# Optimization experiments

Hardware: AMD Instinct MI355X
Metric: run time of the kernel (lower is better)

## Reference

```python
import jax, jax.numpy as jnp
import numpy as np

B, Q, K, C, H = 4, 1024, 1024, 1024, 16
L = C            # latent_dim (== in_dim per module construction)
CH = L // H      # head_dim = 64


def _ln(x, w, b):
    m = jnp.mean(x, -1, keepdims=True)
    v = jnp.mean((x - m) ** 2, -1, keepdims=True)
    return (x - m) * jax.lax.rsqrt(v + 1e-5) * w + b


def setup_inputs() -> dict:
    key = jax.random.key(0)
    ks = jax.random.split(key, 16)
    s = 0.02
    return {
        "queries": jax.random.normal(ks[0], (B, Q, C), jnp.float32),
        "contexts": jax.random.normal(ks[1], (B, K, C), jnp.float32),
        "queries_hidden": jax.random.normal(ks[2], (B, Q, L), jnp.float32),
        "sa_norm_w": jnp.ones((C,), jnp.float32),
        "sa_norm_b": jnp.zeros((C,), jnp.float32),
        "sa_qkv_w": jax.random.normal(ks[3], (C, 2 * L + C), jnp.float32) * s,
        "sa_out_w": jax.random.normal(ks[4], (C, C), jnp.float32) * s,
        "sa_out_b": jnp.zeros((C,), jnp.float32),
        "ca_norm_w": jnp.ones((C,), jnp.float32),
        "ca_norm_b": jnp.zeros((C,), jnp.float32),
        "gru_w_ih": jax.random.normal(ks[5], (3 * L, C), jnp.float32) * s,
        "gru_w_hh": jax.random.normal(ks[6], (3 * L, L), jnp.float32) * s,
        "gru_b_ih": jnp.zeros((3 * L,), jnp.float32),
        "gru_b_hh": jnp.zeros((3 * L,), jnp.float32),
        "ca_k_w": jax.random.normal(ks[7], (C, L), jnp.float32) * s,
        "ca_v_w": jax.random.normal(ks[8], (C, C), jnp.float32) * s,
        "ca_out_w": jax.random.normal(ks[9], (C, C), jnp.float32) * s,
        "ca_out_b": jnp.zeros((C,), jnp.float32),
        "ln1_w": jnp.ones((C,), jnp.float32),
        "ln1_b": jnp.zeros((C,), jnp.float32),
        "lin1_w": jax.random.normal(ks[10], (C, 2 * C), jnp.float32) * s,
        "ln2_w": jnp.ones((2 * C,), jnp.float32),
        "ln2_b": jnp.zeros((2 * C,), jnp.float32),
        "lin2_w": jax.random.normal(ks[11], (2 * C, C), jnp.float32) * s,
    }


def reference(queries, contexts, queries_hidden,
              sa_norm_w, sa_norm_b, sa_qkv_w, sa_out_w, sa_out_b,
              ca_norm_w, ca_norm_b, gru_w_ih, gru_w_hh, gru_b_ih, gru_b_hh,
              ca_k_w, ca_v_w, ca_out_w, ca_out_b,
              ln1_w, ln1_b, lin1_w, ln2_w, ln2_b, lin2_w):
    scale = 1.0 / jnp.sqrt(jnp.asarray(C, queries.dtype))

    # ---- SelfAttention (pre-norm, residual) ----
    xn = _ln(queries, sa_norm_w, sa_norm_b)
    qkv = (xn @ sa_qkv_w).reshape(B, Q, H, -1)          # [B,Q,H, 2*CH + C/H]
    q, k, v = jnp.split(qkv, [CH, 2 * CH], axis=-1)
    e = jnp.einsum('nqhc,nkhc->nhqk', q, k) * scale
    a = jax.nn.softmax(e, axis=-1)
    o = jnp.einsum('nhqk,nkhc->nqhc', a, v).reshape(B, Q, C)
    x = o @ sa_out_w + sa_out_b + queries

    # ---- AttentionDynamicQuery (GRU-updated queries, cross-attn) ----
    x_pre = x
    xn = _ln(x, ca_norm_w, ca_norm_b)
    xf = xn.reshape(B * Q, C)
    hf = queries_hidden.reshape(B * Q, L)
    gi = xf @ gru_w_ih.T + gru_b_ih                     # [BQ, 3L]
    gh = hf @ gru_w_hh.T + gru_b_hh
    gir, giz, gin = jnp.split(gi, 3, axis=-1)
    ghr, ghz, ghn = jnp.split(gh, 3, axis=-1)
    r = jax.nn.sigmoid(gir + ghr)
    z = jax.nn.sigmoid(giz + ghz)
    n = jnp.tanh(gin + r * ghn)
    h = (1.0 - z) * n + z * hf                          # PyTorch GRUCell update
    qh = h.reshape(B, Q, H, CH)                         # new queries_hidden

    kk = (contexts @ ca_k_w).reshape(B, K, H, CH)
    vv = (contexts @ ca_v_w).reshape(B, K, H, C // H)
    energy = jnp.einsum('nqhc,nkhc->nhqk', qh, kk)      # returned UNscaled
    att = jax.nn.softmax(energy * scale, axis=-1)
    o = jnp.einsum('nhqk,nkhc->nqhc', att, vv).reshape(B, Q, C)
    x = o @ ca_out_w + ca_out_b + x_pre

    # ---- MLP: LN -> SiLU -> Linear -> LN -> SiLU -> Linear, residual ----
    m = jax.nn.silu(_ln(x, ln1_w, ln1_b)) @ lin1_w
    m = jax.nn.silu(_ln(m, ln2_w, ln2_b)) @ lin2_w
    out = x + m                                         # dropout(p=0) = identity
    return (out, energy, qh)
```

## Files before the change

kernel.cpp:

```cpp
#include <hip/hip_runtime.h>
#include <hip/hip_bf16.h>
#include <math.h>

static constexpr float SCALE = 0.03125f;

typedef __attribute__((ext_vector_type(4))) float f32x4;
typedef __attribute__((ext_vector_type(8))) __bf16 bf16x8;
typedef __attribute__((ext_vector_type(4))) __bf16 bf16x4;

__device__ __forceinline__ void g2l16(const void* g, void* l) {
  __builtin_amdgcn_global_load_lds(
      (const __attribute__((address_space(1))) unsigned int*)g,
      (__attribute__((address_space(3))) unsigned int*)l,
      16, 0, 0);
}

__global__ __launch_bounds__(256) void prep_all(
    const float* __restrict__ sa_qkv_w, const float* __restrict__ ca_k_w,
    const float* __restrict__ ca_v_w, const float* __restrict__ sa_out_w,
    const float* __restrict__ ca_out_w, const float* __restrict__ lin1_w,
    const float* __restrict__ lin2_w, const float* __restrict__ gru_w_ih,
    const float* __restrict__ gru_w_hh, const float* __restrict__ qhid,
    const float* __restrict__ contexts,
    __bf16* __restrict__ qkvT, __bf16* __restrict__ kT, __bf16* __restrict__ vT,
    __bf16* __restrict__ saoT, __bf16* __restrict__ caoT, __bf16* __restrict__ lin1T,
    __bf16* __restrict__ lin2T, __bf16* __restrict__ ihB, __bf16* __restrict__ hhB,
    __bf16* __restrict__ qhB, __bf16* __restrict__ ctxB) {
  int bid = blockIdx.x;
  int t = threadIdx.x;
  if (bid >= 2816) {
    const float* csrc; __bf16* cdst; int cbase;
    if (bid < 4352)      { csrc = gru_w_ih; cdst = ihB;  cbase = 2816; }
    else if (bid < 5888) { csrc = gru_w_hh; cdst = hhB;  cbase = 4352; }
    else if (bid < 7936) { csrc = qhid;     cdst = qhB;  cbase = 5888; }
    else                 { csrc = contexts; cdst = ctxB; cbase = 7936; }
    size_t idx = ((size_t)(bid - cbase) * 256 + t) * 8;
    float4 a = *(const float4*)(csrc + idx);
    float4 b = *(const float4*)(csrc + idx + 4);
    bf16x8 o = {(__bf16)a.x,(__bf16)a.y,(__bf16)a.z,(__bf16)a.w,
                (__bf16)b.x,(__bf16)b.y,(__bf16)b.z,(__bf16)b.w};
    *(bf16x8*)(cdst + idx) = o;
    return;
  }
  const float* src; __bf16* dst; int Kd, N, base;
  if (bid < 768)       { src = sa_qkv_w; dst = qkvT;  Kd = 1024; N = 3072; base = 0; }
  else if (bid < 1024) { src = ca_k_w;   dst = kT;    Kd = 1024; N = 1024; base = 768; }
  else if (bid < 1280) { src = ca_v_w;   dst = vT;    Kd = 1024; N = 1024; base = 1024; }
  else if (bid < 1536) { src = sa_out_w; dst = saoT;  Kd = 1024; N = 1024; base = 1280; }
  else if (bid < 1792) { src = ca_out_w; dst = caoT;  Kd = 1024; N = 1024; base = 1536; }
  else if (bid < 2304) { src = lin1_w;   dst = lin1T; Kd = 1024; N = 2048; base = 1792; }
  else                 { src = lin2_w;   dst = lin2T; Kd = 2048; N = 1024; base = 2304; }
  int tid = bid - base;
  int ntx = N >> 6;
  int n0 = (tid % ntx) * 64, k0 = (tid / ntx) * 64;
  __shared__ float tile[64][65];
  #pragma unroll
  for (int i = 0; i < 16; ++i) {
    int idx = i * 256 + t; int r = idx >> 6, c = idx & 63;
    tile[r][c] = src[(size_t)(k0 + r) * N + n0 + c];
  }
  __syncthreads();
  #pragma unroll
  for (int i = 0; i < 16; ++i) {
    int idx = i * 256 + t; int r = idx >> 6, c = idx & 63;
    dst[(size_t)(n0 + r) * Kd + k0 + c] = (__bf16)tile[c][r];
  }
}

template <int NV>
__global__ __launch_bounds__(256) void ln_bf16(
    const float* __restrict__ xf, const __bf16* __restrict__ xb,
    const float* __restrict__ w, const float* __restrict__ b,
    __bf16* __restrict__ out, int silu) {
  const int D = NV * 1024;
  int row = blockIdx.x, t = threadIdx.x;
  float vals[NV * 4];
  float s = 0.f, s2 = 0.f;
  #pragma unroll
  for (int i = 0; i < NV; ++i) {
    int c = (i * 256 + t) * 4;
    float4 v;
    if (xf) {
      v = *(const float4*)(xf + (size_t)row * D + c);
    } else {
      bf16x4 vb = *(const bf16x4*)(xb + (size_t)row * D + c);
      v = make_float4((float)vb[0], (float)vb[1], (float)vb[2], (float)vb[3]);
    }
    vals[i*4+0] = v.x; vals[i*4+1] = v.y; vals[i*4+2] = v.z; vals[i*4+3] = v.w;
    s += v.x + v.y + v.z + v.w;
    s2 += v.x*v.x + v.y*v.y + v.z*v.z + v.w*v.w;
  }
  __shared__ float red[256], red2[256];
  red[t] = s; red2[t] = s2;
  __syncthreads();
  for (int off = 128; off > 0; off >>= 1) {
    if (t < off) { red[t] += red[t + off]; red2[t] += red2[t + off]; }
    __syncthreads();
  }
  float mean = red[0] / D;
  float var = red2[0] / D - mean * mean;
  float rs = rsqrtf(var + 1e-5f);
  #pragma unroll
  for (int i = 0; i < NV; ++i) {
    int c = (i * 256 + t) * 4;
    bf16x4 o;
    #pragma unroll
    for (int j = 0; j < 4; ++j) {
      float v = (vals[i*4+j] - mean) * rs * w[c+j] + b[c+j];
      if (silu) v = v / (1.f + __expf(-v));
      o[j] = (__bf16)v;
    }
    *(bf16x4*)(out + (size_t)row * D + c) = o;
  }
}

__global__ __launch_bounds__(256) void gemm_bf16(
    const __bf16* __restrict__ A, long long lda,
    const __bf16* __restrict__ B, long long ldb,
    float* __restrict__ outF, __bf16* __restrict__ outB, long long ldc,
    const float* __restrict__ bias, const float* __restrict__ res, int K) {
  __shared__ __bf16 Asm[128 * 64];
  __shared__ __bf16 Bsm[128 * 64];
  int nwg = gridDim.x * gridDim.y;
  int orig = blockIdx.y * gridDim.x + blockIdx.x;
  int swz = (orig & 7) * (nwg >> 3) + (orig >> 3);
  int bm = (swz / gridDim.x) * 128, bn = (swz % gridDim.x) * 128;
  int t = threadIdx.x;
  int lane = t & 63, w = t >> 6;
  int l15 = lane & 15, kg = lane >> 4;
  int wm = (w >> 1) * 64, wn = (w & 1) * 64;

  f32x4 acc[4][4];
  #pragma unroll
  for (int i = 0; i < 4; ++i)
    #pragma unroll
    for (int j = 0; j < 4; ++j) acc[i][j] = (f32x4)(0.0f);

  const __bf16* ga[4]; const __bf16* gb[4];
  __bf16* la[4]; __bf16* lb[4];
  #pragma unroll
  for (int i = 0; i < 4; ++i) {
    int slot = i * 256 + t;
    int row = slot >> 3, s = slot & 7;
    int sx = s ^ (row & 7);
    ga[i] = A + (size_t)(bm + row) * lda + (sx << 3);
    gb[i] = B + (size_t)(bn + row) * ldb + (sx << 3);
    int base = (i * 256 + w * 64) << 3;
    la[i] = Asm + base;
    lb[i] = Bsm + base;
  }

  for (int k0 = 0; k0 < K; k0 += 64) {
    #pragma unroll
    for (int i = 0; i < 4; ++i) g2l16(ga[i] + k0, la[i]);
    #pragma unroll
    for (int i = 0; i < 4; ++i) g2l16(gb[i] + k0, lb[i]);
    asm volatile("s_waitcnt vmcnt(0)" ::: "memory");
    __syncthreads();
    #pragma unroll
    for (int kk = 0; kk < 2; ++kk) {
      bf16x8 af[4], bfr[4];
      #pragma unroll
      for (int mi = 0; mi < 4; ++mi) {
        int row = wm + mi * 16 + l15;
        int ks = kk * 4 + kg;
        af[mi] = *(const bf16x8*)(Asm + row * 64 + ((ks ^ (row & 7)) << 3));
      }
      #pragma unroll
      for (int ni = 0; ni < 4; ++ni) {
        int row = wn + ni * 16 + l15;
        int ks = kk * 4 + kg;
        bfr[ni] = *(const bf16x8*)(Bsm + row * 64 + ((ks ^ (row & 7)) << 3));
      }
      #pragma unroll
      for (int mi = 0; mi < 4; ++mi)
        #pragma unroll
        for (int ni = 0; ni < 4; ++ni)
          acc[mi][ni] = __builtin_amdgcn_mfma_f32_16x16x32_bf16(
              af[mi], bfr[ni], acc[mi][ni], 0, 0, 0);
    }
    __syncthreads();
  }

  #pragma unroll
  for (int mi = 0; mi < 4; ++mi) {
    #pragma unroll
    for (int ni = 0; ni < 4; ++ni) {
      int rbase = bm + wm + mi * 16 + kg * 4;
      int c = bn + wn + ni * 16 + l15;
      #pragma unroll
      for (int r = 0; r < 4; ++r) {
        float val = acc[mi][ni][r];
        if (bias) val += bias[c];
        size_t off = (size_t)(rbase + r) * ldc + c;
        if (res) val += res[off];
        if (outF) outF[off] = val;
        if (outB) outB[off] = (__bf16)val;
      }
    }
  }
}

__global__ __launch_bounds__(256) void vtrans(
    const __bf16* __restrict__ V, long long v_sb, long long v_sh, int v_sm,
    __bf16* __restrict__ VT) {
  __shared__ __bf16 tile[64][72];
  int g = blockIdx.y, b = g >> 4, h = g & 15;
  int k0 = blockIdx.x * 64;
  const __bf16* Vb = V + (size_t)b * v_sb + (size_t)h * v_sh;
  int t = threadIdx.x;
  #pragma unroll
  for (int i = 0; i < 2; ++i) {
    int idx = i * 256 + t;
    int k = idx >> 3, dc = (idx & 7) * 8;
    bf16x8 v = *(const bf16x8*)(Vb + (size_t)(k0 + k) * v_sm + dc);
    #pragma unroll
    for (int j = 0; j < 8; ++j) tile[dc + j][k] = v[j];
  }
  __syncthreads();
  #pragma unroll
  for (int i = 0; i < 2; ++i) {
    int idx = i * 256 + t;
    int d = idx >> 3, kc = (idx & 7) * 8;
    bf16x8 v;
    #pragma unroll
    for (int j = 0; j < 8; ++j) v[j] = tile[d][kc + j];
    *(bf16x8*)(VT + ((size_t)g * 64 + d) * 1024 + k0 + kc) = v;
  }
}

__global__ __launch_bounds__(256) void flash_attn(
    const __bf16* __restrict__ Qb, long long q_sb, long long q_sh, int q_sm,
    const __bf16* __restrict__ Kb, long long k_sb, long long k_sh, int k_sm,
    const __bf16* __restrict__ VT, __bf16* __restrict__ Ob,
    float* __restrict__ energyOut, float scale) {
  __shared__ __bf16 Ksm[64 * 64];
  __shared__ __bf16 Vsm[64 * 64];
  __shared__ __bf16 Psm[128 * 64];
  __shared__ float corr_l[128];
  __shared__ float l_l[128];
  int g = blockIdx.y, b = g >> 4, h = g & 15;
  int qt = blockIdx.x * 128;
  const __bf16* Qg = Qb + (size_t)b * q_sb + (size_t)h * q_sh;
  const __bf16* Kg = Kb + (size_t)b * k_sb + (size_t)h * k_sh;
  const __bf16* Vg = VT + (size_t)g * 65536;
  int t = threadIdx.x, lane = t & 63, w = t >> 6;
  int l15 = lane & 15, kg = lane >> 4;
  int wq = w * 32;

  bf16x8 qf[2][2];
  #pragma unroll
  for (int nq = 0; nq < 2; ++nq)
    #pragma unroll
    for (int kk = 0; kk < 2; ++kk)
      qf[nq][kk] = *(const bf16x8*)(
          Qg + (size_t)(qt + wq + nq * 16 + l15) * q_sm + kk * 32 + kg * 8);

  f32x4 acc_o[2][4];
  #pragma unroll
  for (int i = 0; i < 2; ++i)
    #pragma unroll
    for (int j = 0; j < 4; ++j) acc_o[i][j] = (f32x4)(0.0f);
  float m_run[2] = {-1e30f, -1e30f};
  float l_run[2] = {0.f, 0.f};

  const __bf16* gK[2]; const __bf16* gV[2];
  __bf16 *lK[2], *lV[2];
  #pragma unroll
  for (int i = 0; i < 2; ++i) {
    int slot = i * 256 + t;
    int row = slot >> 3, s = slot & 7, sx = s ^ (row & 7);
    gK[i] = Kg + (size_t)row * k_sm + (sx << 3);
    gV[i] = Vg + (size_t)row * 1024 + (sx << 3);
    lK[i] = Ksm + ((i * 256 + w * 64) << 3);
    lV[i] = Vsm + ((i * 256 + w * 64) << 3);
  }

  for (int kv0 = 0; kv0 < 1024; kv0 += 64) {
    #pragma unroll
    for (int i = 0; i < 2; ++i) g2l16(gK[i] + (size_t)kv0 * k_sm, lK[i]);
    #pragma unroll
    for (int i = 0; i < 2; ++i) g2l16(gV[i] + kv0, lV[i]);
    asm volatile("s_waitcnt vmcnt(0)" ::: "memory");
    __syncthreads();

    f32x4 accs[4][2];
    #pragma unroll
    for (int i = 0; i < 4; ++i)
      #pragma unroll
      for (int j = 0; j < 2; ++j) accs[i][j] = (f32x4)(0.0f);
    #pragma unroll
    for (int tt = 0; tt < 4; ++tt) {
      bf16x8 kf[2];
      #pragma unroll
      for (int kk = 0; kk < 2; ++kk) {
        int row = tt * 16 + l15;
        int ks = kk * 4 + kg;
        kf[kk] = *(const bf16x8*)(Ksm + row * 64 + ((ks ^ (row & 7)) << 3));
      }
      #pragma unroll
      for (int nq = 0; nq < 2; ++nq)
        #pragma unroll
        for (int kk = 0; kk < 2; ++kk)
          accs[tt][nq] = __builtin_amdgcn_mfma_f32_16x16x32_bf16(
              kf[kk], qf[nq][kk], accs[tt][nq], 0, 0, 0);
    }

    if (energyOut) {
      float* eg = energyOut + ((size_t)g << 20);
      #pragma unroll
      for (int nq = 0; nq < 2; ++nq) {
        int q = qt + wq + nq * 16 + l15;
        #pragma unroll
        for (int tt = 0; tt < 4; ++tt)
          *(f32x4*)(eg + (size_t)q * 1024 + kv0 + tt * 16 + kg * 4) = accs[tt][nq];
      }
    }

    #pragma unroll
    for (int nq = 0; nq < 2; ++nq) {
      float tmax = -1e30f;
      #pragma unroll
      for (int tt = 0; tt < 4; ++tt)
        #pragma unroll
        for (int r = 0; r < 4; ++r) tmax = fmaxf(tmax, accs[tt][nq][r]);
      tmax *= scale;
      tmax = fmaxf(tmax, __shfl_xor(tmax, 16));
      tmax = fmaxf(tmax, __shfl_xor(tmax, 32));
      float m_new = fmaxf(m_run[nq], tmax);
      float corr = __expf(m_run[nq] - m_new);
      m_run[nq] = m_new;
      int q = wq + nq * 16 + l15;
      float psum = 0.f;
      #pragma unroll
      for (int tt = 0; tt < 4; ++tt) {
        bf16x4 p4;
        #pragma unroll
        for (int r = 0; r < 4; ++r) {
          float p = __expf(accs[tt][nq][r] * scale - m_new);
          psum += p;
          p4[r] = (__bf16)p;
        }
        int kvs = (tt * 16 + kg * 4) ^ ((q & 7) << 3);
        *(bf16x4*)(Psm + q * 64 + kvs) = p4;
      }
      psum += __shfl_xor(psum, 16);
      psum += __shfl_xor(psum, 32);
      l_run[nq] = l_run[nq] * corr + psum;
      if (kg == 0) corr_l[q] = corr;
    }
    __syncthreads();

    #pragma unroll
    for (int mq = 0; mq < 2; ++mq) {
      f32x4 c4 = *(const f32x4*)&corr_l[wq + mq * 16 + kg * 4];
      #pragma unroll
      for (int nd = 0; nd < 4; ++nd)
        #pragma unroll
        for (int r = 0; r < 4; ++r) acc_o[mq][nd][r] *= c4[r];
    }
    #pragma unroll
    for (int kk = 0; kk < 2; ++kk) {
      bf16x8 pf[2], vf[4];
      #pragma unroll
      for (int mq = 0; mq < 2; ++mq) {
        int row = wq + mq * 16 + l15;
        int kvs = (kk * 32 + kg * 8) ^ ((row & 7) << 3);
        pf[mq] = *(const bf16x8*)(Psm + row * 64 + kvs);
      }
      #pragma unroll
      for (int nd = 0; nd < 4; ++nd) {
        int vrow = nd * 16 + l15;
        vf[nd] = *(const bf16x8*)(Vsm + vrow * 64 + (((kk * 4 + kg) ^ (vrow & 7)) << 3));
      }
      #pragma unroll
      for (int mq = 0; mq < 2; ++mq)
        #pragma unroll
        for (int nd = 0; nd < 4; ++nd)
          acc_o[mq][nd] = __builtin_amdgcn_mfma_f32_16x16x32_bf16(
              pf[mq], vf[nd], acc_o[mq][nd], 0, 0, 0);
    }
    __syncthreads();
  }

  #pragma unroll
  for (int nq = 0; nq < 2; ++nq)
    if (kg == 0) l_l[wq + nq * 16 + l15] = l_run[nq];
  __syncthreads();

  #pragma unroll
  for (int mq = 0; mq < 2; ++mq) {
    f32x4 lv = *(const f32x4*)&l_l[wq + mq * 16 + kg * 4];
    #pragma unroll
    for (int nd = 0; nd < 4; ++nd) {
      int col = h * 64 + nd * 16 + l15;
      #pragma unroll
      for (int r = 0; r < 4; ++r) {
        int qrow = qt + wq + mq * 16 + kg * 4 + r;
        Ob[(size_t)(b * 1024 + qrow) * 1024 + col] = (__bf16)(acc_o[mq][nd][r] / lv[r]);
      }
    }
  }
}

__global__ __launch_bounds__(256) void gru_kernel(
    const __bf16* __restrict__ gi, const __bf16* __restrict__ gh,
    const float* __restrict__ hf, float* __restrict__ qh, __bf16* __restrict__ qhb) {
  size_t e0 = ((size_t)blockIdx.x * 256 + threadIdx.x) * 8;
  int row = (int)(e0 >> 10), col = (int)(e0 & 1023);
  size_t base = (size_t)row * 3072 + col;
  bf16x8 vir = *(const bf16x8*)(gi + base);
  bf16x8 viz = *(const bf16x8*)(gi + base + 1024);
  bf16x8 vin = *(const bf16x8*)(gi + base + 2048);
  bf16x8 vhr = *(const bf16x8*)(gh + base);
  bf16x8 vhz = *(const bf16x8*)(gh + base + 1024);
  bf16x8 vhn = *(const bf16x8*)(gh + base + 2048);
  float4 h0 = *(const float4*)(hf + e0);
  float4 h1 = *(const float4*)(hf + e0 + 4);
  float hv[8] = {h0.x, h0.y, h0.z, h0.w, h1.x, h1.y, h1.z, h1.w};
  float q[8];
  #pragma unroll
  for (int j = 0; j < 8; ++j) {
    float r = 1.f / (1.f + __expf(-((float)vir[j] + (float)vhr[j])));
    float z = 1.f / (1.f + __expf(-((float)viz[j] + (float)vhz[j])));
    float n = tanhf((float)vin[j] + r * (float)vhn[j]);
    q[j] = (1.f - z) * n + z * hv[j];
  }
  *(float4*)(qh + e0)     = make_float4(q[0], q[1], q[2], q[3]);
  *(float4*)(qh + e0 + 4) = make_float4(q[4], q[5], q[6], q[7]);
  bf16x8 qb;
  #pragma unroll
  for (int j = 0; j < 8; ++j) qb[j] = (__bf16)q[j];
  *(bf16x8*)(qhb + e0) = qb;
}

extern "C" void kernel_launch(void* const* d_in, const int* in_sizes, int n_in,
                              void* d_out, int out_size, void* d_ws, size_t ws_size,
                              hipStream_t stream) {
  (void)in_sizes; (void)n_in; (void)out_size; (void)ws_size;
  const float* queries   = (const float*)d_in[0];
  const float* contexts  = (const float*)d_in[1];
  const float* qhid      = (const float*)d_in[2];
  const float* sa_norm_w = (const float*)d_in[3];
  const float* sa_norm_b = (const float*)d_in[4];
  const float* sa_qkv_w  = (const float*)d_in[5];
  const float* sa_out_w  = (const float*)d_in[6];
  const float* sa_out_b  = (const float*)d_in[7];
  const float* ca_norm_w = (const float*)d_in[8];
  const float* ca_norm_b = (const float*)d_in[9];
  const float* gru_w_ih  = (const float*)d_in[10];
  const float* gru_w_hh  = (const float*)d_in[11];
  const float* gru_b_ih  = (const float*)d_in[12];
  const float* gru_b_hh  = (const float*)d_in[13];
  const float* ca_k_w    = (const float*)d_in[14];
  const float* ca_v_w    = (const float*)d_in[15];
  const float* ca_out_w  = (const float*)d_in[16];
  const float* ca_out_b  = (const float*)d_in[17];
  const float* ln1_w     = (const float*)d_in[18];
  const float* ln1_b     = (const float*)d_in[19];
  const float* lin1_w    = (const float*)d_in[20];
  const float* ln2_w     = (const float*)d_in[21];
  const float* ln2_b     = (const float*)d_in[22];
  const float* lin2_w    = (const float*)d_in[23];

  float* out0   = (float*)d_out;
  float* energy = out0 + (size_t)4194304;
  float* qh_out = out0 + (size_t)71303168;

  const size_t MM = 1u << 20;
  float* ws = (float*)d_ws;
  float*  X     = ws;
  float*  X2    = ws + 4 * MM;
  __bf16* M1B    = (__bf16*)(ws + 9 * MM);
  __bf16* XN_b   = (__bf16*)(ws + 17 * MM);
  __bf16* QHID_b = (__bf16*)(ws + 19 * MM);
  __bf16* CTX_b  = (__bf16*)(ws + 21 * MM);
  __bf16* O_b    = (__bf16*)(ws + 23 * MM);
  __bf16* VT_b   = (__bf16*)(ws + 25 * MM);
  __bf16* QKV_b  = (__bf16*)(ws + 27 * MM);
  __bf16* KV_b   = (__bf16*)(ws + 27 * MM);
  __bf16* LN2_b  = (__bf16*)(ws);
  __bf16* qkvT   = (__bf16*)(ws + 33 * MM);
  __bf16* ihB    = (__bf16*)(ws + 34 * MM + MM / 2);
  __bf16* hhB    = (__bf16*)(ws + 36 * MM);
  __bf16* kT     = (__bf16*)(ws + 37 * MM + MM / 2);
  __bf16* vT     = (__bf16*)(ws + 38 * MM);
  __bf16* saoT   = (__bf16*)(ws + 38 * MM + MM / 2);
  __bf16* caoT   = (__bf16*)(ws + 39 * MM);
  __bf16* lin1T  = (__bf16*)(ws + 39 * MM + MM / 2);
  __bf16* lin2T  = (__bf16*)(ws + 40 * MM + MM / 2);
  __bf16* GI_b = (__bf16*)energy;
  __bf16* GH_b = (__bf16*)(energy + 6 * MM);

  const long long QKV_SB = 1024LL * 3072;
  const long long KV_SB  = 1024LL * 2048;

  prep_all<<<9984, 256, 0, stream>>>(
      sa_qkv_w, ca_k_w, ca_v_w, sa_out_w, ca_out_w, lin1_w, lin2_w,
      gru_w_ih, gru_w_hh, qhid, contexts,
      qkvT, kT, vT, saoT, caoT, lin1T, lin2T, ihB, hhB, QHID_b, CTX_b);

  ln_bf16<1><<<4096, 256, 0, stream>>>(queries, nullptr, sa_norm_w, sa_norm_b, XN_b, 0);
  gemm_bf16<<<dim3(24, 32), 256, 0, stream>>>(
      XN_b, 1024, qkvT, 1024, nullptr, QKV_b, 3072, nullptr, nullptr, 1024);
  vtrans<<<dim3(16, 64), 256, 0, stream>>>(QKV_b + 128, QKV_SB, 192, 3072, VT_b);
  flash_attn<<<dim3(8, 64), 256, 0, stream>>>(
      QKV_b, QKV_SB, 192, 3072, QKV_b + 64, QKV_SB, 192, 3072,
      VT_b, O_b, nullptr, SCALE);
  gemm_bf16<<<dim3(8, 32), 256, 0, stream>>>(
      O_b, 1024, saoT, 1024, X, nullptr, 1024, sa_out_b, queries, 1024);

  ln_bf16<1><<<4096, 256, 0, stream>>>(X, nullptr, ca_norm_w, ca_norm_b, XN_b, 0);
  gemm_bf16<<<dim3(24, 32), 256, 0, stream>>>(
      XN_b, 1024, ihB, 1024, nullptr, GI_b, 3072, gru_b_ih, nullptr, 1024);
  gemm_bf16<<<dim3(24, 32), 256, 0, stream>>>(
      QHID_b, 1024, hhB, 1024, nullptr, GH_b, 3072, gru_b_hh, nullptr, 1024);
  gru_kernel<<<2048, 256, 0, stream>>>(GI_b, GH_b, qhid, qh_out, QHID_b );

  gemm_bf16<<<dim3(16, 32), 256, 0, stream>>>(
      CTX_b, 1024, kT, 1024, nullptr, KV_b, 2048, nullptr, nullptr, 1024);
  vtrans<<<dim3(16, 64), 256, 0, stream>>>(KV_b + 1024, KV_SB, 64, 2048, VT_b);
  flash_attn<<<dim3(8, 64), 256, 0, stream>>>(
      QHID_b, 1024LL * 1024, 64, 1024, KV_b, KV_SB, 64, 2048,
      VT_b, O_b, energy, SCALE);
  gemm_bf16<<<dim3(8, 32), 256, 0, stream>>>(
      O_b, 1024, caoT, 1024, X2, nullptr, 1024, ca_out_b, X, 1024);

  ln_bf16<1><<<4096, 256, 0, stream>>>(X2, nullptr, ln1_w, ln1_b, XN_b, 1);
  gemm_bf16<<<dim3(16, 32), 256, 0, stream>>>(
      XN_b, 1024, lin1T, 1024, nullptr, M1B, 2048, nullptr, nullptr, 1024);
  ln_bf16<2><<<4096, 256, 0, stream>>>(nullptr, M1B, ln2_w, ln2_b, LN2_b, 1);
  gemm_bf16<<<dim3(8, 32), 256, 0, stream>>>(
      LN2_b, 2048, lin2T, 2048, out0, nullptr, 1024, nullptr, X2, 2048);
}
```

Before: 654.0 us.

## Triple-buffer flash attention K/V, merge independent GEMMs, and use shuffle reductions in LN

Flash attention now prefetches K/V tiles two steps ahead into a three-slot LDS ring, using counted vmcnt waits and a single barrier per step in place of full drains. It also raises wave priority around the MFMA sections and writes the energy output with nontemporal stores. Independent GEMMs (sa_out with gru_hh, gru_ih with the context K/V projection) are merged into one dual-problem launch to fill the GPU and cut launch count. LayerNorm switches its reduction from a shared-memory tree to wave shuffles. The vmcnt counts are hand-tuned to the issue order, so any change in how loads are issued could break correctness.

```diff
diff --git a/kernel.cpp b/kernel.cpp
--- a/kernel.cpp
+++ b/kernel.cpp
@@ -90,15 +90,19 @@
     s += v.x + v.y + v.z + v.w;
     s2 += v.x*v.x + v.y*v.y + v.z*v.z + v.w*v.w;
   }
-  __shared__ float red[256], red2[256];
-  red[t] = s; red2[t] = s2;
+  #pragma unroll
+  for (int off = 32; off > 0; off >>= 1) {
+    s += __shfl_xor(s, off);
+    s2 += __shfl_xor(s2, off);
+  }
+  __shared__ float red[4], red2[4];
+  int wv = t >> 6;
+  if ((t & 63) == 0) { red[wv] = s; red2[wv] = s2; }
   __syncthreads();
-  for (int off = 128; off > 0; off >>= 1) {
-    if (t < off) { red[t] += red[t + off]; red2[t] += red2[t + off]; }
-    __syncthreads();
-  }
-  float mean = red[0] / D;
-  float var = red2[0] / D - mean * mean;
+  float S  = red[0] + red[1] + red[2] + red[3];
+  float S2 = red2[0] + red2[1] + red2[2] + red2[3];
+  float mean = S / D;
+  float var = S2 / D - mean * mean;
   float rs = rsqrtf(var + 1e-5f);
   #pragma unroll
   for (int i = 0; i < NV; ++i) {
@@ -114,17 +118,13 @@
   }
 }
 
-__global__ __launch_bounds__(256) void gemm_bf16(
+__device__ __forceinline__ void gemm_body(
+    __bf16* Asm, __bf16* Bsm,
     const __bf16* __restrict__ A, long long lda,
     const __bf16* __restrict__ B, long long ldb,
     float* __restrict__ outF, __bf16* __restrict__ outB, long long ldc,
-    const float* __restrict__ bias, const float* __restrict__ res, int K) {
-  __shared__ __bf16 Asm[128 * 64];
-  __shared__ __bf16 Bsm[128 * 64];
-  int nwg = gridDim.x * gridDim.y;
-  int orig = blockIdx.y * gridDim.x + blockIdx.x;
-  int swz = (orig & 7) * (nwg >> 3) + (orig >> 3);
-  int bm = (swz / gridDim.x) * 128, bn = (swz % gridDim.x) * 128;
+    const float* __restrict__ bias, const float* __restrict__ res,
+    int K, int bm, int bn) {
   int t = threadIdx.x;
   int lane = t & 63, w = t >> 6;
   int l15 = lane & 15, kg = lane >> 4;
@@ -201,6 +201,41 @@
   }
 }
 
+__global__ __launch_bounds__(256) void gemm_bf16(
+    const __bf16* __restrict__ A, long long lda,
+    const __bf16* __restrict__ B, long long ldb,
+    float* __restrict__ outF, __bf16* __restrict__ outB, long long ldc,
+    const float* __restrict__ bias, const float* __restrict__ res, int K) {
+  __shared__ __bf16 sm[2 * 8192];
+  int nwg = gridDim.x * gridDim.y;
+  int orig = blockIdx.y * gridDim.x + blockIdx.x;
+  int swz = (orig & 7) * (nwg >> 3) + (orig >> 3);
+  gemm_body(sm, sm + 8192, A, lda, B, ldb, outF, outB, ldc, bias, res, K,
+            (swz / gridDim.x) * 128, (swz % gridDim.x) * 128);
+}
+
+__global__ __launch_bounds__(256) void gemm_dual(
+    const __bf16* __restrict__ A0, long long lda0, const __bf16* __restrict__ B0, long long ldb0,
+    float* __restrict__ oF0, __bf16* __restrict__ oB0, long long ldc0,
+    const float* __restrict__ bias0, const float* __restrict__ res0, int K0, int gx0, int nb0,
+    const __bf16* __restrict__ A1, long long lda1, const __bf16* __restrict__ B1, long long ldb1,
+    float* __restrict__ oF1, __bf16* __restrict__ oB1, long long ldc1,
+    const float* __restrict__ bias1, const float* __restrict__ res1, int K1, int gx1) {
+  __shared__ __bf16 sm[2 * 8192];
+  int bid = blockIdx.x;
+  if (bid < nb0) {
+    int swz = (bid & 7) * (nb0 >> 3) + (bid >> 3);
+    gemm_body(sm, sm + 8192, A0, lda0, B0, ldb0, oF0, oB0, ldc0, bias0, res0, K0,
+              (swz / gx0) * 128, (swz % gx0) * 128);
+  } else {
+    int b = bid - nb0;
+    int nb1 = gridDim.x - nb0;
+    int swz = (b & 7) * (nb1 >> 3) + (b >> 3);
+    gemm_body(sm, sm + 8192, A1, lda1, B1, ldb1, oF1, oB1, ldc1, bias1, res1, K1,
+              (swz / gx1) * 128, (swz % gx1) * 128);
+  }
+}
+
 __global__ __launch_bounds__(256) void vtrans(
     const __bf16* __restrict__ V, long long v_sb, long long v_sh, int v_sm,
     __bf16* __restrict__ VT) {
@@ -229,13 +264,14 @@
   }
 }
 
+template <int E>
 __global__ __launch_bounds__(256) void flash_attn(
     const __bf16* __restrict__ Qb, long long q_sb, long long q_sh, int q_sm,
     const __bf16* __restrict__ Kb, long long k_sb, long long k_sh, int k_sm,
     const __bf16* __restrict__ VT, __bf16* __restrict__ Ob,
     float* __restrict__ energyOut, float scale) {
-  __shared__ __bf16 Ksm[64 * 64];
-  __shared__ __bf16 Vsm[64 * 64];
+  __shared__ __bf16 Ksm[3][4096];
+  __shared__ __bf16 Vsm[3][4096];
   __shared__ __bf16 Psm[128 * 64];
   __shared__ float corr_l[128];
   __shared__ float l_l[128];
@@ -265,30 +301,56 @@
   float l_run[2] = {0.f, 0.f};
 
   const __bf16* gK[2]; const __bf16* gV[2];
-  __bf16 *lK[2], *lV[2];
+  int lo[2];
   #pragma unroll
   for (int i = 0; i < 2; ++i) {
     int slot = i * 256 + t;
     int row = slot >> 3, s = slot & 7, sx = s ^ (row & 7);
     gK[i] = Kg + (size_t)row * k_sm + (sx << 3);
     gV[i] = Vg + (size_t)row * 1024 + (sx << 3);
-    lK[i] = Ksm + ((i * 256 + w * 64) << 3);
-    lV[i] = Vsm + ((i * 256 + w * 64) << 3);
-  }
-
-  for (int kv0 = 0; kv0 < 1024; kv0 += 64) {
-    #pragma unroll
-    for (int i = 0; i < 2; ++i) g2l16(gK[i] + (size_t)kv0 * k_sm, lK[i]);
-    #pragma unroll
-    for (int i = 0; i < 2; ++i) g2l16(gV[i] + kv0, lV[i]);
-    asm volatile("s_waitcnt vmcnt(0)" ::: "memory");
-    __syncthreads();
+    lo[i] = (i * 256 + w * 64) << 3;
+  }
+
+  #pragma unroll
+  for (int i = 0; i < 2; ++i) g2l16(gK[i], &Ksm[0][lo[i]]);
+  #pragma unroll
+  for (int i = 0; i < 2; ++i) g2l16(gV[i], &Vsm[0][lo[i]]);
+  #pragma unroll
+  for (int i = 0; i < 2; ++i) g2l16(gK[i] + (size_t)64 * k_sm, &Ksm[1][lo[i]]);
+  #pragma unroll
+  for (int i = 0; i < 2; ++i) g2l16(gV[i] + 64, &Vsm[1][lo[i]]);
+
+  int rb = 0;
+  for (int kvt = 0; kvt < 16; ++kvt) {
+    if (E) {
+      if (kvt == 0)       asm volatile("s_waitcnt vmcnt(4)" ::: "memory");
+      else if (kvt == 1)  asm volatile("s_waitcnt vmcnt(12)" ::: "memory");
+      else if (kvt == 15) asm volatile("s_waitcnt vmcnt(16)" ::: "memory");
+      else                asm volatile("s_waitcnt vmcnt(20)" ::: "memory");
+    } else {
+      if (kvt == 15)      asm volatile("s_waitcnt vmcnt(0)" ::: "memory");
+      else                asm volatile("s_waitcnt vmcnt(4)" ::: "memory");
+    }
+    __builtin_amdgcn_s_barrier();
+    __builtin_amdgcn_sched_barrier(0);
+
+    if (kvt < 14) {
+      int sbuf = rb >= 1 ? rb - 1 : rb + 2;
+      size_t ko = (size_t)(kvt + 2) << 6;
+      #pragma unroll
+      for (int i = 0; i < 2; ++i) g2l16(gK[i] + ko * k_sm, &Ksm[sbuf][lo[i]]);
+      #pragma unroll
+      for (int i = 0; i < 2; ++i) g2l16(gV[i] + ko, &Vsm[sbuf][lo[i]]);
+    }
+    const __bf16* Ks = Ksm[rb];
+    const __bf16* Vs = Vsm[rb];
 
     f32x4 accs[4][2];
     #pragma unroll
     for (int i = 0; i < 4; ++i)
       #pragma unroll
       for (int j = 0; j < 2; ++j) accs[i][j] = (f32x4)(0.0f);
+    __builtin_amdgcn_s_setprio(1);
     #pragma unroll
     for (int tt = 0; tt < 4; ++tt) {
       bf16x8 kf[2];
@@ -296,7 +358,7 @@
       for (int kk = 0; kk < 2; ++kk) {
         int row = tt * 16 + l15;
         int ks = kk * 4 + kg;
-        kf[kk] = *(const bf16x8*)(Ksm + row * 64 + ((ks ^ (row & 7)) << 3));
+        kf[kk] = *(const bf16x8*)(Ks + row * 64 + ((ks ^ (row & 7)) << 3));
       }
       #pragma unroll
       for (int nq = 0; nq < 2; ++nq)
@@ -305,15 +367,18 @@
           accs[tt][nq] = __builtin_amdgcn_mfma_f32_16x16x32_bf16(
               kf[kk], qf[nq][kk], accs[tt][nq], 0, 0, 0);
     }
-
-    if (energyOut) {
+    __builtin_amdgcn_s_setprio(0);
+
+    if (E) {
+      int kv0 = kvt << 6;
       float* eg = energyOut + ((size_t)g << 20);
       #pragma unroll
       for (int nq = 0; nq < 2; ++nq) {
         int q = qt + wq + nq * 16 + l15;
         #pragma unroll
         for (int tt = 0; tt < 4; ++tt)
-          *(f32x4*)(eg + (size_t)q * 1024 + kv0 + tt * 16 + kg * 4) = accs[tt][nq];
+          __builtin_nontemporal_store(
+              accs[tt][nq], (f32x4*)(eg + (size_t)q * 1024 + kv0 + tt * 16 + kg * 4));
       }
     }
 
@@ -349,7 +414,6 @@
       l_run[nq] = l_run[nq] * corr + psum;
       if (kg == 0) corr_l[q] = corr;
     }
-    __syncthreads();
 
     #pragma unroll
     for (int mq = 0; mq < 2; ++mq) {
@@ -359,6 +423,7 @@
         #pragma unroll
         for (int r = 0; r < 4; ++r) acc_o[mq][nd][r] *= c4[r];
     }
+    __builtin_amdgcn_s_setprio(1);
     #pragma unroll
     for (int kk = 0; kk < 2; ++kk) {
       bf16x8 pf[2], vf[4];
@@ -371,7 +436,7 @@
       #pragma unroll
       for (int nd = 0; nd < 4; ++nd) {
         int vrow = nd * 16 + l15;
-        vf[nd] = *(const bf16x8*)(Vsm + vrow * 64 + (((kk * 4 + kg) ^ (vrow & 7)) << 3));
+        vf[nd] = *(const bf16x8*)(Vs + vrow * 64 + (((kk * 4 + kg) ^ (vrow & 7)) << 3));
       }
       #pragma unroll
       for (int mq = 0; mq < 2; ++mq)
@@ -380,7 +445,8 @@
           acc_o[mq][nd] = __builtin_amdgcn_mfma_f32_16x16x32_bf16(
               pf[mq], vf[nd], acc_o[mq][nd], 0, 0, 0);
     }
-    __syncthreads();
+    __builtin_amdgcn_s_setprio(0);
+    rb = rb == 2 ? 0 : rb + 1;
   }
 
   #pragma unroll
@@ -504,23 +570,21 @@
   gemm_bf16<<<dim3(24, 32), 256, 0, stream>>>(
       XN_b, 1024, qkvT, 1024, nullptr, QKV_b, 3072, nullptr, nullptr, 1024);
   vtrans<<<dim3(16, 64), 256, 0, stream>>>(QKV_b + 128, QKV_SB, 192, 3072, VT_b);
-  flash_attn<<<dim3(8, 64), 256, 0, stream>>>(
+  flash_attn<0><<<dim3(8, 64), 256, 0, stream>>>(
       QKV_b, QKV_SB, 192, 3072, QKV_b + 64, QKV_SB, 192, 3072,
       VT_b, O_b, nullptr, SCALE);
-  gemm_bf16<<<dim3(8, 32), 256, 0, stream>>>(
-      O_b, 1024, saoT, 1024, X, nullptr, 1024, sa_out_b, queries, 1024);
+  gemm_dual<<<1024, 256, 0, stream>>>(
+      O_b, 1024, saoT, 1024, X, nullptr, 1024, sa_out_b, queries, 1024, 8, 256,
+      QHID_b, 1024, hhB, 1024, nullptr, GH_b, 3072, gru_b_hh, nullptr, 1024, 24);
 
   ln_bf16<1><<<4096, 256, 0, stream>>>(X, nullptr, ca_norm_w, ca_norm_b, XN_b, 0);
-  gemm_bf16<<<dim3(24, 32), 256, 0, stream>>>(
-      XN_b, 1024, ihB, 1024, nullptr, GI_b, 3072, gru_b_ih, nullptr, 1024);
-  gemm_bf16<<<dim3(24, 32), 256, 0, stream>>>(
-      QHID_b, 1024, hhB, 1024, nullptr, GH_b, 3072, gru_b_hh, nullptr, 1024);
+  gemm_dual<<<1280, 256, 0, stream>>>(
+      XN_b, 1024, ihB, 1024, nullptr, GI_b, 3072, gru_b_ih, nullptr, 1024, 24, 768,
+      CTX_b, 1024, kT, 1024, nullptr, KV_b, 2048, nullptr, nullptr, 1024, 16);
   gru_kernel<<<2048, 256, 0, stream>>>(GI_b, GH_b, qhid, qh_out, QHID_b );
 
-  gemm_bf16<<<dim3(16, 32), 256, 0, stream>>>(
-      CTX_b, 1024, kT, 1024, nullptr, KV_b, 2048, nullptr, nullptr, 1024);
   vtrans<<<dim3(16, 64), 256, 0, stream>>>(KV_b + 1024, KV_SB, 64, 2048, VT_b);
-  flash_attn<<<dim3(8, 64), 256, 0, stream>>>(
+  flash_attn<1><<<dim3(8, 64), 256, 0, stream>>>(
       QHID_b, 1024LL * 1024, 64, 1024, KV_b, KV_SB, 64, 2048,
       VT_b, O_b, energy, SCALE);
   gemm_bf16<<<dim3(8, 32), 256, 0, stream>>>(
```

Result: faster. 623.7 us (-4.6%).
